# Performance work log

Hardware: AMD Instinct MI355X
Metric: run time of the kernel (lower is better)

Reference implementation:

```python
import jax, jax.numpy as jnp
import numpy as np

N_NODES = 100000
N_EDGES = 3200000
D_FEAT = 512
D_HID = 64
N_CLS = 40


def setup_inputs() -> dict:
    key = jax.random.key(0)
    k1, k2, k3, k4, k5, k6, k7 = jax.random.split(key, 7)
    x = jax.random.normal(k1, (N_NODES, D_FEAT), dtype=jnp.float32)
    edge_index = jax.random.randint(k2, (2, N_EDGES), 0, N_NODES, dtype=jnp.int64)
    edge_weight = jax.random.uniform(k3, (N_EDGES,), dtype=jnp.float32)
    # GCNConv params (glorot-ish scale)
    W1 = jax.random.normal(k4, (D_FEAT, D_HID), dtype=jnp.float32) / np.sqrt(D_FEAT)
    b1 = jnp.zeros((D_HID,), dtype=jnp.float32)
    W2 = jax.random.normal(k5, (D_HID, N_CLS), dtype=jnp.float32) / np.sqrt(D_HID)
    b2 = jnp.zeros((N_CLS,), dtype=jnp.float32)
    return {"x": x, "edge_index": edge_index, "edge_weight": edge_weight,
            "W1": W1, "b1": b1, "W2": W2, "b2": b2}


def _gcn_norm(edge_index, edge_weight, num_nodes):
    # add self-loops with weight 1 (PyG gcn_norm default)
    loop = jnp.arange(num_nodes, dtype=edge_index.dtype)
    row = jnp.concatenate([edge_index[0], loop])
    col = jnp.concatenate([edge_index[1], loop])
    ew = jnp.concatenate([edge_weight, jnp.ones((num_nodes,), edge_weight.dtype)])
    deg = jax.ops.segment_sum(ew, col, num_segments=num_nodes)  # in-degree (weighted)
    dinv = jnp.where(deg > 0, jax.lax.rsqrt(deg), 0.0)
    norm = dinv[row] * ew * dinv[col]
    return row, col, norm


def _gcn_conv(x, row, col, norm, W, b, num_nodes):
    x = x @ W  # linear first (out_channels small): [N, out]
    msg = norm[:, None] * x[row]            # gather + scale: [E+N, out]
    out = jax.ops.segment_sum(msg, col, num_segments=num_nodes)  # scatter-add
    return out + b


def reference(x, edge_index, edge_weight, W1, b1, W2, b2):
    n = x.shape[0]
    row, col, norm = _gcn_norm(edge_index, edge_weight, n)
    h = jax.nn.relu(_gcn_conv(x, row, col, norm, W1, b1, n))
    # dropout omitted (eval-mode determinism for correctness baseline)
    logits = _gcn_conv(h, row, col, norm, W2, b2, n)
    return jax.nn.log_softmax(logits, axis=1)
```

## Files before the change

### kernel.cpp

```cpp
#include <hip/hip_runtime.h>
#include <math.h>

#define N_NODES 100000
#define N_EDGES 3200000
#define D_FEAT  512
#define D_HID   64
#define N_CLS   40
#define NBKT    391
#define NBLKA   256
#define EPB     (N_EDGES / NBLKA)

typedef __attribute__((ext_vector_type(8))) short short8;
typedef __attribute__((ext_vector_type(4))) float floatx4;

static __device__ __forceinline__ unsigned short f2bf(float f) {
    unsigned u = __float_as_uint(f);
    unsigned r = (u + 0x7FFFu + ((u >> 16) & 1u)) >> 16;
    return (unsigned short)r;
}
static __device__ __forceinline__ float bf2f(unsigned short h) {
    return __uint_as_float(((unsigned)h) << 16);
}
static __device__ __forceinline__ short8 pack_bf16x8(float4 a, float4 b) {
    short8 r;
    r[0] = (short)f2bf(a.x); r[1] = (short)f2bf(a.y);
    r[2] = (short)f2bf(a.z); r[3] = (short)f2bf(a.w);
    r[4] = (short)f2bf(b.x); r[5] = (short)f2bf(b.y);
    r[6] = (short)f2bf(b.z); r[7] = (short)f2bf(b.w);
    return r;
}


__global__ __launch_bounds__(256) void k_histA(const int* __restrict__ ei,
                                               int* __restrict__ mat) {
    __shared__ int hist[NBKT];
    const int tid = threadIdx.x, blk = blockIdx.x;
    for (int i = tid; i < NBKT; i += 256) hist[i] = 0;
    __syncthreads();
    const int e0 = blk * EPB, e1 = e0 + EPB;
    for (int e = e0 + tid; e < e1; e += 256)
        atomicAdd(&hist[ei[N_EDGES + e] >> 8], 1);
    __syncthreads();
    for (int i = tid; i < NBKT; i += 256) mat[i * NBLKA + blk] = hist[i];
}


__global__ __launch_bounds__(256) void k_scanRows(int* __restrict__ mat,
                                                  int* __restrict__ total) {
    __shared__ int s[256];
    const int tid = threadIdx.x, bin = blockIdx.x;
    int v = mat[bin * NBLKA + tid];
    s[tid] = v;
    __syncthreads();
    for (int off = 1; off < 256; off <<= 1) {
        int t = (tid >= off) ? s[tid - off] : 0;
        __syncthreads();
        s[tid] += t;
        __syncthreads();
    }
    mat[bin * NBLKA + tid] = s[tid] - v;
    if (tid == 255) total[bin] = s[255];
}


__global__ __launch_bounds__(512) void k_scanTot(const int* __restrict__ total,
                                                 int* __restrict__ cbase) {
    __shared__ int s[512];
    const int tid = threadIdx.x;
    int v = (tid < NBKT) ? total[tid] : 0;
    s[tid] = v;
    __syncthreads();
    for (int off = 1; off < 512; off <<= 1) {
        int t = (tid >= off) ? s[tid - off] : 0;
        __syncthreads();
        s[tid] += t;
        __syncthreads();
    }
    if (tid <= NBKT) cbase[tid] = s[tid] - v;
}


__global__ __launch_bounds__(256) void k_scatterB(const int* __restrict__ ei,
                                                  const float* __restrict__ ew,
                                                  const int* __restrict__ mat,
                                                  const int* __restrict__ cbase,
                                                  int2* __restrict__ tmpA,
                                                  unsigned char* __restrict__ tmpD) {
    __shared__ int cur[NBKT];
    const int tid = threadIdx.x, blk = blockIdx.x;
    for (int i = tid; i < NBKT; i += 256)
        cur[i] = cbase[i] + mat[i * NBLKA + blk];
    __syncthreads();
    const int e0 = blk * EPB, e1 = e0 + EPB;
    for (int e = e0 + tid; e < e1; e += 256) {
        int r = ei[e];
        int c = ei[N_EDGES + e];
        int slot = atomicAdd(&cur[c >> 8], 1);
        tmpA[slot] = make_int2(r, __float_as_int(ew[e]));
        tmpD[slot] = (unsigned char)(c & 255);
    }
}


__global__ __launch_bounds__(256) void k_bucketC(const int* __restrict__ cbase,
                                                 const int2* __restrict__ tmpA,
                                                 const unsigned char* __restrict__ tmpD,
                                                 int2* __restrict__ csr,
                                                 int* __restrict__ cnt,
                                                 int* __restrict__ base,
                                                 float* __restrict__ dinv) {
    __shared__ int   c_cnt[256];
    __shared__ float c_deg[256];
    __shared__ int   c_scan[256];
    __shared__ int   c_cur[256];
    __shared__ float c_dnv[256];
    const int tid = threadIdx.x, b = blockIdx.x;
    const int s = cbase[b], e = cbase[b + 1];
    c_cnt[tid] = 0;
    c_deg[tid] = 0.f;
    __syncthreads();
    for (int j = s + tid; j < e; j += 256) {
        int d = tmpD[j];
        atomicAdd(&c_cnt[d], 1);
        atomicAdd(&c_deg[d], __int_as_float(tmpA[j].y));
    }
    __syncthreads();
    int v = c_cnt[tid];
    c_scan[tid] = v;
    __syncthreads();
    for (int off = 1; off < 256; off <<= 1) {
        int t = (tid >= off) ? c_scan[tid - off] : 0;
        __syncthreads();
        c_scan[tid] += t;
        __syncthreads();
    }
    int excl = c_scan[tid] - v;
    c_cur[tid] = excl;
    float dv = rsqrtf(1.0f + c_deg[tid]);
    c_dnv[tid] = dv;
    int node = b * 256 + tid;
    if (node < N_NODES) {
        cnt[node]  = v;
        base[node] = s + excl;
        dinv[node] = dv;
    }
    __syncthreads();
    for (int j = s + tid; j < e; j += 256) {
        int d = tmpD[j];
        int2 p = tmpA[j];
        int slot = atomicAdd(&c_cur[d], 1);
        csr[s + slot] = make_int2(p.x, __float_as_int(__int_as_float(p.y) * c_dnv[d]));
    }
}


__global__ __launch_bounds__(256) void k_norm(int2* __restrict__ csr,
                                              const float* __restrict__ dinv) {
    int i = blockIdx.x * 256 + threadIdx.x;
    int2 p = csr[i];
    p.y = __float_as_int(__int_as_float(p.y) * dinv[p.x]);
    csr[i] = p;
}


__global__ __launch_bounds__(256) void k_gemm1(const float* __restrict__ x,
                                               const float* __restrict__ W1,
                                               unsigned short* __restrict__ hpre) {
    __shared__ __align__(16) short Wt[64 * 512];
    const int tid = threadIdx.x;

    {
        const int c  = tid & 63;
        const int kb = (tid >> 6) * 128;
        const int sw = (c & 7) << 3;
        for (int kk = 0; kk < 128; kk += 8) {
            short8 v;
#pragma unroll
            for (int j = 0; j < 8; j++)
                v[j] = (short)f2bf(W1[(size_t)(kb + kk + j) * D_HID + c]);
            *(short8*)&Wt[c * 512 + ((kb + kk) ^ sw)] = v;
        }
    }
    __syncthreads();

    const int widx = blockIdx.x * 4 + (tid >> 6);
    if (widx >= N_NODES / 16) return;
    const int lane = tid & 63;
    const int q  = lane >> 4;
    const int cn = lane & 15;
    const int r0 = widx * 16;
    const int sw = (cn & 7) << 3;

    floatx4 acc[4] = {{0,0,0,0},{0,0,0,0},{0,0,0,0},{0,0,0,0}};
    const float* xp = x + (size_t)(r0 + cn) * D_FEAT + q * 8;

#pragma unroll 4
    for (int k0 = 0; k0 < D_FEAT; k0 += 32) {
        float4 xa = *(const float4*)(xp + k0);
        float4 xb = *(const float4*)(xp + k0 + 4);
        short8 a = pack_bf16x8(xa, xb);
#pragma unroll
        for (int ct = 0; ct < 4; ct++) {
            short8 b = *(const short8*)&Wt[(ct * 16 + cn) * 512 + ((k0 + q * 8) ^ sw)];
            acc[ct] = __builtin_amdgcn_mfma_f32_16x16x32_bf16(a, b, acc[ct], 0, 0, 0);
        }
    }

#pragma unroll
    for (int ct = 0; ct < 4; ct++)
#pragma unroll
        for (int i = 0; i < 4; i++)
            hpre[(size_t)(r0 + q * 4 + i) * D_HID + ct * 16 + cn] = f2bf(acc[ct][i]);
}


__global__ __launch_bounds__(256) void k_gather1(const int* __restrict__ base,
                                                 const int* __restrict__ cnt,
                                                 const int2* __restrict__ csr,
                                                 const unsigned char* __restrict__ hpreB,
                                                 const float* __restrict__ dinv,
                                                 const float* __restrict__ b1,
                                                 const float* __restrict__ W2,
                                                 unsigned short* __restrict__ z16) {
    __shared__ float hs[4][64];
    __shared__ int2  eds[4][64];
    const int lane = threadIdx.x & 63;
    const int w = threadIdx.x >> 6;
    const int n = blockIdx.x * 4 + w;
    const int s = base[n], e = s + cnt[n];
    const float dn = dinv[n];
    const int q = lane & 31;
    const int vsel = lane >> 5;
    const unsigned laneoff = (unsigned)q << 2;

    float accx[4] = {0.f, 0.f, 0.f, 0.f};
    float accy[4] = {0.f, 0.f, 0.f, 0.f};
    {
        unsigned pv = *(const unsigned*)(hpreB + (((unsigned)n) << 7) + laneoff);
        float dn2 = vsel ? 0.f : dn * dn;
        accx[0] = dn2 * __uint_as_float(pv << 16);
        accy[0] = dn2 * __uint_as_float(pv & 0xffff0000u);
    }

    for (int c = s; c < e; c += 64) {
        int idx = c + lane;
        int2 ed = csr[idx < e ? idx : (e - 1)];
        if (idx >= e) ed.y = 0;
        eds[w][lane] = ed;
        int nc = e - c; if (nc > 64) nc = 64;
        for (int j = 0; j < nc; j += 16) {
            int2 ep[8]; unsigned pv[8];
#pragma unroll
            for (int p = 0; p < 8; p++)
                ep[p] = eds[w][j + 2 * p + vsel];
#pragma unroll
            for (int p = 0; p < 8; p++)
                pv[p] = *(const unsigned*)(hpreB + (((unsigned)ep[p].x) << 7) + laneoff);
#pragma unroll
            for (int p = 0; p < 8; p++) {
                float wj = __int_as_float(ep[p].y);
                accx[p & 3] = fmaf(wj, __uint_as_float(pv[p] << 16), accx[p & 3]);
                accy[p & 3] = fmaf(wj, __uint_as_float(pv[p] & 0xffff0000u), accy[p & 3]);
            }
        }
    }

    float tx = (accx[0] + accx[1]) + (accx[2] + accx[3]);
    float ty = (accy[0] + accy[1]) + (accy[2] + accy[3]);
    tx += __shfl_xor(tx, 32, 64);
    ty += __shfl_xor(ty, 32, 64);
    if (lane < 32) {
        float h0 = tx + b1[2 * lane];
        float h1 = ty + b1[2 * lane + 1];
        hs[w][2 * lane]     = h0 > 0.f ? h0 : 0.f;
        hs[w][2 * lane + 1] = h1 > 0.f ? h1 : 0.f;
    }
    float a2 = 0.f;
    if (lane < N_CLS) {
#pragma unroll
        for (int k = 0; k < D_HID; k += 4) {
            float4 hv = *(const float4*)&hs[w][k];
            a2 += hv.x * W2[(k    ) * N_CLS + lane] + hv.y * W2[(k + 1) * N_CLS + lane]
                + hv.z * W2[(k + 2) * N_CLS + lane] + hv.w * W2[(k + 3) * N_CLS + lane];
        }
    }
    z16[(size_t)n * D_HID + lane] = (lane < N_CLS) ? f2bf(a2) : 0;
}


__global__ __launch_bounds__(256) void k_gather2_lsm(const int* __restrict__ base,
                                                     const int* __restrict__ cnt,
                                                     const int2* __restrict__ csr,
                                                     const unsigned char* __restrict__ zB,
                                                     const float* __restrict__ dinv,
                                                     const float* __restrict__ b2,
                                                     float* __restrict__ out) {
    __shared__ int2 eds[4][64];
    const int lane = threadIdx.x & 63;
    const int w = threadIdx.x >> 6;
    const int n = blockIdx.x * 4 + w;
    const int s = base[n], e = s + cnt[n];
    const float dn = dinv[n];
    const int q = lane & 31;
    const int vsel = lane >> 5;
    const unsigned laneoff = (unsigned)q << 2;

    float accx[4] = {0.f, 0.f, 0.f, 0.f};
    float accy[4] = {0.f, 0.f, 0.f, 0.f};
    {
        unsigned pv = *(const unsigned*)(zB + (((unsigned)n) << 7) + laneoff);
        float dn2 = vsel ? 0.f : dn * dn;
        accx[0] = dn2 * __uint_as_float(pv << 16);
        accy[0] = dn2 * __uint_as_float(pv & 0xffff0000u);
    }

    for (int c = s; c < e; c += 64) {
        int idx = c + lane;
        int2 ed = csr[idx < e ? idx : (e - 1)];
        if (idx >= e) ed.y = 0;
        eds[w][lane] = ed;
        int nc = e - c; if (nc > 64) nc = 64;
        for (int j = 0; j < nc; j += 16) {
            int2 ep[8]; unsigned pv[8];
#pragma unroll
            for (int p = 0; p < 8; p++)
                ep[p] = eds[w][j + 2 * p + vsel];
#pragma unroll
            for (int p = 0; p < 8; p++)
                pv[p] = *(const unsigned*)(zB + (((unsigned)ep[p].x) << 7) + laneoff);
#pragma unroll
            for (int p = 0; p < 8; p++) {
                float wj = __int_as_float(ep[p].y);
                accx[p & 3] = fmaf(wj, __uint_as_float(pv[p] << 16), accx[p & 3]);
                accy[p & 3] = fmaf(wj, __uint_as_float(pv[p] & 0xffff0000u), accy[p & 3]);
            }
        }
    }

    float tx = (accx[0] + accx[1]) + (accx[2] + accx[3]);
    float ty = (accy[0] + accy[1]) + (accy[2] + accy[3]);
    tx += __shfl_xor(tx, 32, 64);
    ty += __shfl_xor(ty, 32, 64);

    const bool act2 = q < (N_CLS / 2);
    float lg0 = 0.f, lg1 = 0.f;
    if (act2) {
        lg0 = tx + b2[2 * q];
        lg1 = ty + b2[2 * q + 1];
    }
    float m = act2 ? fmaxf(lg0, lg1) : -INFINITY;
    for (int off = 16; off; off >>= 1) m = fmaxf(m, __shfl_xor(m, off, 64));
    float ev = act2 ? (expf(lg0 - m) + expf(lg1 - m)) : 0.f;
    float sum = ev;
    for (int off = 16; off; off >>= 1) sum += __shfl_xor(sum, off, 64);
    float ls = logf(sum);
    if (lane < (N_CLS / 2)) {
        float2 o;
        o.x = lg0 - m - ls;
        o.y = lg1 - m - ls;
        *(float2*)(out + (size_t)n * N_CLS + 2 * lane) = o;
    }
}


extern "C" void kernel_launch(void* const* d_in, const int* in_sizes, int n_in,
                              void* d_out, int out_size, void* d_ws, size_t ws_size,
                              hipStream_t stream) {
    const float* x  = (const float*)d_in[0];
    const int*   ei = (const int*)d_in[1];
    const float* ew = (const float*)d_in[2];
    const float* W1 = (const float*)d_in[3];
    const float* b1 = (const float*)d_in[4];
    const float* W2 = (const float*)d_in[5];
    const float* b2 = (const float*)d_in[6];
    float* out = (float*)d_out;

    int* ws = (int*)d_ws;
    int2*          csr  = (int2*)ws;
    int2*          tmpA = (int2*)(ws + 2 * (size_t)N_EDGES);
    unsigned char* tmpD = (unsigned char*)(ws + 4 * (size_t)N_EDGES);
    int*   mat   = ws + 4 * (size_t)N_EDGES + N_EDGES / 4;
    int*   total = mat + NBKT * NBLKA;
    int*   cbase = total + NBKT;
    unsigned short* hpre = (unsigned short*)tmpA;
    unsigned short* z16  = hpre + (size_t)N_NODES * D_HID;
    int*   cnt  = ws + 16000000;
    int*   base = cnt + N_NODES;
    float* dinv = (float*)(base + N_NODES);

    k_histA   <<<NBLKA, 256, 0, stream>>>(ei, mat);
    k_scanRows<<<NBKT,  256, 0, stream>>>(mat, total);
    k_scanTot <<<1,     512, 0, stream>>>(total, cbase);
    k_scatterB<<<NBLKA, 256, 0, stream>>>(ei, ew, mat, cbase, tmpA, tmpD);
    k_bucketC <<<NBKT,  256, 0, stream>>>(cbase, tmpA, tmpD, csr, cnt, base, dinv);
    k_norm    <<<N_EDGES / 256, 256, 0, stream>>>(csr, dinv);
    k_gemm1   <<<(N_NODES / 16 + 3) / 4, 256, 0, stream>>>(x, W1, hpre);
    k_gather1 <<<N_NODES / 4, 256, 0, stream>>>(base, cnt, csr,
                                                (const unsigned char*)hpre, dinv, b1, W2, z16);
    k_gather2_lsm<<<N_NODES / 4, 256, 0, stream>>>(base, cnt, csr,
                                                   (const unsigned char*)z16, dinv, b2, out);
}
```

Measured before the change: 655.7 us.

## Compute degrees with global atomics in histogram pass and drop normalization kernel

Weighted in-degree is now accumulated with global float atomics during the column histogram pass, and dinv is computed in a small separate kernel. Full edge normalization (ew*dinv[r]*dinv[c]) is applied in the scatter pass, which removes the separate k_norm pass over the CSR and the degree accumulation in the bucket kernel. Edge loads in the gather kernels use nontemporal loads. This adds 3.2M global float atomics, two tiny launches and random dinv reads in the scatter, and float atomic ordering makes degree sums nondeterministic.

New measurement: 784.1 us. 1.2x slower.

```diff
diff --git a/kernel.cpp b/kernel.cpp
--- a/kernel.cpp
+++ b/kernel.cpp
@@ -29,19 +29,42 @@
     r[6] = (short)f2bf(b.z); r[7] = (short)f2bf(b.w);
     return r;
 }
+static __device__ __forceinline__ int2 nt_load_int2(const int2* p) {
+    long long v = __builtin_nontemporal_load((const long long*)p);
+    int2 r; r.x = (int)(unsigned)(v & 0xffffffffll); r.y = (int)(v >> 32);
+    return r;
+}
+
+
+__global__ __launch_bounds__(256) void k_zero(float* __restrict__ deg) {
+    int i = blockIdx.x * 256 + threadIdx.x;
+    if (i < N_NODES) deg[i] = 0.f;
+}
 
 
 __global__ __launch_bounds__(256) void k_histA(const int* __restrict__ ei,
-                                               int* __restrict__ mat) {
+                                               const float* __restrict__ ew,
+                                               int* __restrict__ mat,
+                                               float* __restrict__ deg) {
     __shared__ int hist[NBKT];
     const int tid = threadIdx.x, blk = blockIdx.x;
     for (int i = tid; i < NBKT; i += 256) hist[i] = 0;
     __syncthreads();
     const int e0 = blk * EPB, e1 = e0 + EPB;
-    for (int e = e0 + tid; e < e1; e += 256)
-        atomicAdd(&hist[ei[N_EDGES + e] >> 8], 1);
+    for (int e = e0 + tid; e < e1; e += 256) {
+        int c = ei[N_EDGES + e];
+        atomicAdd(&hist[c >> 8], 1);
+        atomicAdd(&deg[c], ew[e]);
+    }
     __syncthreads();
     for (int i = tid; i < NBKT; i += 256) mat[i * NBLKA + blk] = hist[i];
+}
+
+
+__global__ __launch_bounds__(256) void k_dinv(const float* __restrict__ deg,
+                                              float* __restrict__ dinv) {
+    int i = blockIdx.x * 256 + threadIdx.x;
+    if (i < N_NODES) dinv[i] = rsqrtf(1.0f + deg[i]);
 }
 
 
@@ -84,6 +107,7 @@
                                                   const float* __restrict__ ew,
                                                   const int* __restrict__ mat,
                                                   const int* __restrict__ cbase,
+                                                  const float* __restrict__ dinv,
                                                   int2* __restrict__ tmpA,
                                                   unsigned char* __restrict__ tmpD) {
     __shared__ int cur[NBKT];
@@ -95,8 +119,9 @@
     for (int e = e0 + tid; e < e1; e += 256) {
         int r = ei[e];
         int c = ei[N_EDGES + e];
+        float wn = ew[e] * dinv[r] * dinv[c];
         int slot = atomicAdd(&cur[c >> 8], 1);
-        tmpA[slot] = make_int2(r, __float_as_int(ew[e]));
+        tmpA[slot] = make_int2(r, __float_as_int(wn));
         tmpD[slot] = (unsigned char)(c & 255);
     }
 }
@@ -107,23 +132,16 @@
                                                  const unsigned char* __restrict__ tmpD,
                                                  int2* __restrict__ csr,
                                                  int* __restrict__ cnt,
-                                                 int* __restrict__ base,
-                                                 float* __restrict__ dinv) {
-    __shared__ int   c_cnt[256];
-    __shared__ float c_deg[256];
-    __shared__ int   c_scan[256];
-    __shared__ int   c_cur[256];
-    __shared__ float c_dnv[256];
+                                                 int* __restrict__ base) {
+    __shared__ int c_cnt[256];
+    __shared__ int c_scan[256];
+    __shared__ int c_cur[256];
     const int tid = threadIdx.x, b = blockIdx.x;
     const int s = cbase[b], e = cbase[b + 1];
     c_cnt[tid] = 0;
-    c_deg[tid] = 0.f;
-    __syncthreads();
-    for (int j = s + tid; j < e; j += 256) {
-        int d = tmpD[j];
-        atomicAdd(&c_cnt[d], 1);
-        atomicAdd(&c_deg[d], __int_as_float(tmpA[j].y));
-    }
+    __syncthreads();
+    for (int j = s + tid; j < e; j += 256)
+        atomicAdd(&c_cnt[tmpD[j]], 1);
     __syncthreads();
     int v = c_cnt[tid];
     c_scan[tid] = v;
@@ -136,30 +154,17 @@
     }
     int excl = c_scan[tid] - v;
     c_cur[tid] = excl;
-    float dv = rsqrtf(1.0f + c_deg[tid]);
-    c_dnv[tid] = dv;
     int node = b * 256 + tid;
     if (node < N_NODES) {
         cnt[node]  = v;
         base[node] = s + excl;
-        dinv[node] = dv;
     }
     __syncthreads();
     for (int j = s + tid; j < e; j += 256) {
         int d = tmpD[j];
-        int2 p = tmpA[j];
         int slot = atomicAdd(&c_cur[d], 1);
-        csr[s + slot] = make_int2(p.x, __float_as_int(__int_as_float(p.y) * c_dnv[d]));
-    }
-}
-
-
-__global__ __launch_bounds__(256) void k_norm(int2* __restrict__ csr,
-                                              const float* __restrict__ dinv) {
-    int i = blockIdx.x * 256 + threadIdx.x;
-    int2 p = csr[i];
-    p.y = __float_as_int(__int_as_float(p.y) * dinv[p.x]);
-    csr[i] = p;
+        csr[s + slot] = tmpA[j];
+    }
 }
 
 
@@ -244,7 +249,7 @@
 
     for (int c = s; c < e; c += 64) {
         int idx = c + lane;
-        int2 ed = csr[idx < e ? idx : (e - 1)];
+        int2 ed = nt_load_int2(&csr[idx < e ? idx : (e - 1)]);
         if (idx >= e) ed.y = 0;
         eds[w][lane] = ed;
         int nc = e - c; if (nc > 64) nc = 64;
@@ -316,7 +321,7 @@
 
     for (int c = s; c < e; c += 64) {
         int idx = c + lane;
-        int2 ed = csr[idx < e ? idx : (e - 1)];
+        int2 ed = nt_load_int2(&csr[idx < e ? idx : (e - 1)]);
         if (idx >= e) ed.y = 0;
         eds[w][lane] = ed;
         int nc = e - c; if (nc > 64) nc = 64;
@@ -387,13 +392,15 @@
     int*   cnt  = ws + 16000000;
     int*   base = cnt + N_NODES;
     float* dinv = (float*)(base + N_NODES);
-
-    k_histA   <<<NBLKA, 256, 0, stream>>>(ei, mat);
+    float* deg  = dinv + N_NODES;
+
+    k_zero    <<<NBKT,  256, 0, stream>>>(deg);
+    k_histA   <<<NBLKA, 256, 0, stream>>>(ei, ew, mat, deg);
+    k_dinv    <<<NBKT,  256, 0, stream>>>(deg, dinv);
     k_scanRows<<<NBKT,  256, 0, stream>>>(mat, total);
     k_scanTot <<<1,     512, 0, stream>>>(total, cbase);
-    k_scatterB<<<NBLKA, 256, 0, stream>>>(ei, ew, mat, cbase, tmpA, tmpD);
-    k_bucketC <<<NBKT,  256, 0, stream>>>(cbase, tmpA, tmpD, csr, cnt, base, dinv);
-    k_norm    <<<N_EDGES / 256, 256, 0, stream>>>(csr, dinv);
+    k_scatterB<<<NBLKA, 256, 0, stream>>>(ei, ew, mat, cbase, dinv, tmpA, tmpD);
+    k_bucketC <<<NBKT,  256, 0, stream>>>(cbase, tmpA, tmpD, csr, cnt, base);
     k_gemm1   <<<(N_NODES / 16 + 3) / 4, 256, 0, stream>>>(x, W1, hpre);
     k_gather1 <<<N_NODES / 4, 256, 0, stream>>>(base, cnt, csr,
                                                 (const unsigned char*)hpre, dinv, b1, W2, z16);
```
